# Kernel optimization log

Hardware: AMD Instinct MI355X
Metric: run time of the kernel (lower is better)

## Reference

```python
import jax, jax.numpy as jnp
import numpy as np
import math

N_NODES, N_EDGES, NNZ, D, L = 100000, 20000, 500000, 128, 4
ALPHA, LAMDA = 0.1, 0.5


def setup_inputs() -> dict:
    key = jax.random.key(0)
    ks = jax.random.split(key, 16)
    x = jax.random.normal(ks[0], (N_NODES, D), jnp.float32)
    e = jax.random.normal(ks[1], (N_EDGES, D), jnp.float32)
    nodes = jax.random.randint(ks[2], (NNZ,), 0, N_NODES)
    edges = jnp.sort(jax.random.randint(ks[3], (NNZ,), 0, N_EDGES)).at[-1].set(N_EDGES - 1)
    hyperedge_index = jnp.stack([nodes, edges]).astype(jnp.int32)
    dist_v2e = jax.random.randint(ks[4], (NNZ,), 0, 64).astype(jnp.float32)
    deg_v2e = jax.random.randint(ks[5], (NNZ,), 0, 64).astype(jnp.float32)
    dist_e2v = jax.random.randint(ks[6], (NNZ,), 0, 64).astype(jnp.float32)
    deg_e2v = jax.random.randint(ks[7], (NNZ,), 0, 64).astype(jnp.float32)
    s = 0.05
    W0 = jax.random.normal(ks[8], (D, D), jnp.float32) * s
    b0 = jnp.zeros((D,), jnp.float32)
    Wn = jax.random.normal(ks[9], (L, D, D), jnp.float32) * s
    We = jax.random.normal(ks[10], (L, D, D), jnp.float32) * s
    attn_w = jax.random.normal(ks[11], (L, 2 * D), jnp.float32) * s
    attn_b = jnp.zeros((L,), jnp.float32)
    wd_w = jax.random.normal(ks[12], (L,), jnp.float32) * s
    wd_b = jnp.zeros((L,), jnp.float32)
    wg_w = jax.random.normal(ks[13], (L,), jnp.float32) * s
    wg_b = jnp.zeros((L,), jnp.float32)
    return dict(x=x, e=e, hyperedge_index=hyperedge_index, dist_v2e=dist_v2e,
                deg_v2e=deg_v2e, dist_e2v=dist_e2v, deg_e2v=deg_e2v,
                W0=W0, b0=b0, Wn=Wn, We=We, attn_w=attn_w, attn_b=attn_b,
                wd_w=wd_w, wd_b=wd_b, wg_w=wg_w, wg_b=wg_b)


def _seg_softmax(s, idx, num):
    # numerically-stable scatter_softmax over segments idx
    m = jax.ops.segment_max(s, idx, num_segments=num)
    ex = jnp.exp(s - m[idx])
    den = jax.ops.segment_sum(ex, idx, num_segments=num)
    return ex / den[idx]


def _forward(x, e, hei, dv2e, gv2e, de2v, ge2v, W0, b0, Wn, We, aw, ab, wdw, wdb, wgw, wgb):
    nodes, edges = hei[0], hei[1]
    N, E = x.shape[0], e.shape[0]
    ones = jnp.ones(nodes.shape[0], x.dtype)
    dV = jax.ops.segment_sum(ones, nodes, num_segments=N)
    cnt = jax.ops.segment_sum(ones, edges, num_segments=E)
    dE = jax.ops.segment_sum(dV[nodes], edges, num_segments=E) / jnp.maximum(cnt, 1.0)
    degV = jnp.where(dV > 0, dV ** -0.5, 1.0)[:, None]   # [N,1]
    degE = jnp.where(dE > 0, dE ** -0.5, 1.0)[:, None]   # [E,1]

    x = jax.nn.relu(x @ W0 + b0)
    x0, e0 = x, e
    d = x.shape[1]
    for i in range(L):
        beta = math.log(LAMDA / (i + 1) + 1.0)
        # v2e attention: concat [x[nodes], e[edges]] -> softmax over edge segments
        sx1 = x @ aw[i, :d]; se1 = e @ aw[i, d:]
        s_v2e = sx1[nodes] + se1[edges] + ab[i] + dv2e * wdw[i] + wdb[i] + gv2e * wgw[i] + wgb[i]
        a_v2e = _seg_softmax(s_v2e, edges, E)[:, None]
        # e2v attention (flipped): concat [e[edges], x[nodes]] -> softmax over node segments
        se2 = e @ aw[i, :d]; sx2 = x @ aw[i, d:]
        s_e2v = se2[edges] + sx2[nodes] + ab[i] + de2v * wdw[i] + wdb[i] + ge2v * wgw[i] + wgb[i]
        a_e2v = _seg_softmax(s_e2v, nodes, N)[:, None]

        Xe1 = jax.ops.segment_sum(x[nodes] * a_v2e, edges, num_segments=E) * degE
        Xv1 = jax.ops.segment_sum(Xe1[edges] * a_e2v, nodes, num_segments=N) * degV
        Xv2 = jax.ops.segment_sum(e[edges] * a_e2v, nodes, num_segments=N) * degV
        Xe2 = jax.ops.segment_sum(Xv2[nodes] * a_v2e, edges, num_segments=E) * degE
        xm = (Xv1 + Xv2) * 0.5
        em = (Xe1 + Xe2) * 0.5
        xi = (1 - ALPHA) * xm + ALPHA * x0
        x = (1 - beta) * xi + beta * (xi @ Wn[i])
        ei = (1 - ALPHA) * em + ALPHA * e0
        e = (1 - beta) * ei + beta * (ei @ We[i])
        if i < L - 1:
            x = jax.nn.relu(x)
            e = jax.nn.relu(e)
    return x, e


def reference(x, e, hyperedge_index, dist_v2e, deg_v2e, dist_e2v, deg_e2v,
              W0, b0, Wn, We, attn_w, attn_b, wd_w, wd_b, wg_w, wg_b):
    return _forward(x, e, hyperedge_index, dist_v2e, deg_v2e, dist_e2v, deg_e2v,
                    W0, b0, Wn, We, attn_w, attn_b, wd_w, wd_b, wg_w, wg_b)
```

## Files before the change

kernel.cpp:

```cpp
#include <hip/hip_runtime.h>
#include <hip/hip_fp16.h>
#include <math.h>

#define DD 128
#define SCAN_BLOCKS 256
#define SMAX_CAP 128

typedef _Float16 f16x8 __attribute__((ext_vector_type(8)));
typedef float f32x4 __attribute__((ext_vector_type(4)));

__device__ inline float wave_sum(float v){
#pragma unroll
  for (int m = 32; m >= 1; m >>= 1) v += __shfl_xor(v, m, 64);
  return v;
}
__device__ inline int wave_sum_i(int v){
#pragma unroll
  for (int m = 32; m >= 1; m >>= 1) v += __shfl_xor(v, m, 64);
  return v;
}


__global__ void k_edge_offsets(const int* __restrict__ edges, int nnz, int E,
                               int* __restrict__ eo){
  int e = blockIdx.x * blockDim.x + threadIdx.x;
  if (e > E) return;
  int lo = 0, hi = nnz;
  while (lo < hi){ int mid = (lo + hi) >> 1; if (edges[mid] < e) lo = mid + 1; else hi = mid; }
  eo[e] = lo;
}

__global__ void k_hist(const int* __restrict__ nodes, int nnz, int* __restrict__ dV){
  int k = blockIdx.x * blockDim.x + threadIdx.x;
  if (k < nnz) atomicAdd(&dV[nodes[k]], 1);
}

__global__ __launch_bounds__(256) void k_scan_partial(const int* __restrict__ dV, int N,
                                                      int* __restrict__ part){
  int b = blockIdx.x, t = threadIdx.x;
  int chunk = (N + SCAN_BLOCKS - 1) / SCAN_BLOCKS;
  int s0 = b * chunk, s1 = min(s0 + chunk, N);
  int sum = 0;
  for (int n = s0 + t; n < s1; n += 256) sum += dV[n];
  sum = wave_sum_i(sum);
  __shared__ int wred[4];
  int lane = t & 63, wid = t >> 6;
  if (lane == 0) wred[wid] = sum;
  __syncthreads();
  if (t == 0) part[b] = wred[0] + wred[1] + wred[2] + wred[3];
}

__global__ __launch_bounds__(SCAN_BLOCKS) void k_scan_blocksums(int* __restrict__ part){
  __shared__ int sh[SCAN_BLOCKS];
  int t = threadIdx.x;
  int v = part[t];
  sh[t] = v; __syncthreads();
  for (int off = 1; off < SCAN_BLOCKS; off <<= 1){
    int add = (t >= off) ? sh[t - off] : 0;
    __syncthreads();
    sh[t] += add;
    __syncthreads();
  }
  part[t] = sh[t] - v;
}

__global__ __launch_bounds__(256) void k_scan_apply(const int* __restrict__ dV, int N, int nnz,
    const int* __restrict__ partScan, int* __restrict__ no, int* __restrict__ nfill,
    float* __restrict__ degV){
  int b = blockIdx.x, t = threadIdx.x;
  int chunk = (N + SCAN_BLOCKS - 1) / SCAN_BLOCKS;
  int s0 = b * chunk, s1 = min(s0 + chunk, N);
  int lane = t & 63, wid = t >> 6;
  __shared__ int wtot[4];
  __shared__ int s_run;
  if (t == 0) s_run = partScan[b];
  __syncthreads();
  for (int base = s0; base < s1; base += 256){
    int n = base + t;
    int d = (n < s1) ? dV[n] : 0;
    int v = d;
#pragma unroll
    for (int off = 1; off < 64; off <<= 1){
      int o = __shfl_up(v, off, 64);
      if (lane >= off) v += o;
    }
    if (lane == 63) wtot[wid] = v;
    __syncthreads();
    int run0 = s_run;
    int woff = 0;
    for (int w = 0; w < wid; w++) woff += wtot[w];
    if (n < s1){
      int excl = run0 + woff + v - d;
      no[n] = excl; nfill[n] = excl;
      degV[n] = d > 0 ? 1.0f / sqrtf((float)d) : 1.0f;
    }
    int btot = wtot[0] + wtot[1] + wtot[2] + wtot[3];
    __syncthreads();
    if (t == 0) s_run = run0 + btot;
    __syncthreads();
  }
  if (b == 0 && t == 0) no[N] = nnz;
}

__global__ void k_permpack(const int* __restrict__ nodes, const int* __restrict__ edges,
                           const float* __restrict__ dist, const float* __restrict__ deg,
                           int nnz, int* __restrict__ nfill, float2* __restrict__ pack){
  int k = blockIdx.x * blockDim.x + threadIdx.x;
  if (k < nnz){
    int pos = atomicAdd(&nfill[nodes[k]], 1);
    pack[pos] = make_float2(__int_as_float(edges[k]), dist[k] + 64.f * deg[k]);
  }
}

__global__ void k_edge_deg(const int* __restrict__ nodes, const int* __restrict__ eo, int E,
                           const int* __restrict__ dV, float* __restrict__ degE){
  int e = blockIdx.x * blockDim.x + threadIdx.x;
  if (e >= E) return;
  int b = eo[e], en = eo[e + 1];
  float s = 0.f;
  for (int k = b; k < en; k++) s += (float)dV[nodes[k]];
  float cnt = (float)(en - b);
  float dE = s / fmaxf(cnt, 1.0f);
  degE[e] = dE > 0.f ? 1.0f / sqrtf(dE) : 1.0f;
}

__global__ __launch_bounds__(256) void k_einit(const float2* __restrict__ e_in2,
    const float* __restrict__ aw1, const float* __restrict__ aw2,
    int E, __half2* __restrict__ e0h,
    float* __restrict__ se1, float* __restrict__ se2){
  int wave = threadIdx.x >> 6, lane = threadIdx.x & 63;
  int e = blockIdx.x * 4 + wave;
  if (e >= E) return;
  float2 v = e_in2[(size_t)e * 64 + lane];
  e0h[(size_t)e * 64 + lane] = __floats2half2_rn(v.x, v.y);
  float2 a2v = ((const float2*)aw2)[lane];
  float2 a1v = ((const float2*)aw1)[lane];
  float s1 = v.x * a2v.x + v.y * a2v.y;
  float s2 = v.x * a1v.x + v.y * a1v.y;
  s1 = wave_sum(s1); s2 = wave_sum(s2);
  if (lane == 0){ se1[e] = s1; se2[e] = s2; }
}

__global__ void k_wcast(const float* __restrict__ W0, const float* __restrict__ Wn,
                        const float* __restrict__ We, _Float16* __restrict__ Wt){
  int idx = blockIdx.x * 256 + threadIdx.x;
  if (idx >= 9 * 16384) return;
  int m = idx >> 14, r = idx & 16383;
  int n = r >> 7, k = r & 127;
  float v;
  if (m == 0){
    v = W0[k * 128 + n];
  } else {
    int i = (m <= 4) ? m - 1 : m - 5;
    const float* src = (m <= 4) ? Wn + (size_t)i * 16384 : We + (size_t)i * 16384;
    float beta = logf(0.5f / (float)(i + 1) + 1.0f);
    v = beta * src[k * 128 + n] + ((n == k) ? (1.0f - beta) : 0.f);
  }
  Wt[(size_t)m * 16384 + n * 128 + k] = (_Float16)v;
}


__device__ inline void acc8h(const float4 q, float w, float* a){
  float2 h0 = __half22float2(*(const __half2*)&q.x);
  float2 h1 = __half22float2(*(const __half2*)&q.y);
  float2 h2v = __half22float2(*(const __half2*)&q.z);
  float2 h3 = __half22float2(*(const __half2*)&q.w);
  a[0] += w * h0.x; a[1] += w * h0.y; a[2] += w * h1.x; a[3] += w * h1.y;
  a[4] += w * h2v.x; a[5] += w * h2v.y; a[6] += w * h3.x; a[7] += w * h3.y;
}

__global__ __launch_bounds__(256) void k_sma1(
    const int* __restrict__ nodes, const int* __restrict__ eo,
    const float* __restrict__ sx1, const float* __restrict__ se1,
    const float* __restrict__ dist, const float* __restrict__ deg,
    const float* __restrict__ ab, const float* __restrict__ wdw, const float* __restrict__ wdb,
    const float* __restrict__ wgw, const float* __restrict__ wgb, int li,
    const float* __restrict__ degE, const float4* __restrict__ xh4,
    const _Float16* __restrict__ ehL,
    int E, float* __restrict__ a_v2e, float* __restrict__ esc, _Float16* __restrict__ ETraw){
  __shared__ float lw[4][SMAX_CAP];
  int lane = threadIdx.x & 63;
  int wave = threadIdx.x >> 6;
  int e = blockIdx.x * 4 + wave;
  if (e >= E) return;
  int b = eo[e], en = eo[e + 1];
  int l16 = lane & 15, q16 = lane >> 4;
  if (b >= en){
    if (lane == 0) esc[e] = 0.f;
    if (q16 == 0){
      f16x8 ehv = *(const f16x8*)(ehL + (size_t)e * 128 + 8 * l16);
      f16x8 o0, o1;
#pragma unroll
      for (int q = 0; q < 2; q++){
        o0[4 * q] = (_Float16)0.f; o0[4 * q + 1] = (_Float16)0.f;
        o0[4 * q + 2] = ehv[2 * q]; o0[4 * q + 3] = ehv[2 * q + 1];
        o1[4 * q] = (_Float16)0.f; o1[4 * q + 1] = (_Float16)0.f;
        o1[4 * q + 2] = ehv[2 * q + 4]; o1[4 * q + 3] = ehv[2 * q + 5];
      }
      _Float16* dst = ETraw + (size_t)e * 256 + 16 * l16;
      *(f16x8*)dst = o0; *(f16x8*)(dst + 8) = o1;
    }
    return;
  }
  float base = se1[e] + ab[li] + wdb[li] + wgb[li];
  float wd = wdw[li], wg = wgw[li];
  float m = -INFINITY;
  float sreg[2];
#pragma unroll
  for (int c = 0; c < 2; c++){
    int k = b + lane + 64 * c;
    if (k < en){
      float s = sx1[nodes[k]] + base + dist[k] * wd + deg[k] * wg;
      sreg[c] = s; m = fmaxf(m, s);
    }
  }
  for (int k = b + lane + SMAX_CAP; k < en; k += 64){
    float s = sx1[nodes[k]] + base + dist[k] * wd + deg[k] * wg;
    m = fmaxf(m, s);
  }
#pragma unroll
  for (int mm = 32; mm >= 1; mm >>= 1) m = fmaxf(m, __shfl_xor(m, mm, 64));
  float sum = 0.f;
#pragma unroll
  for (int c = 0; c < 2; c++){
    int k = b + lane + 64 * c;
    if (k < en){
      float ex = __expf(sreg[c] - m);
      a_v2e[k] = ex; lw[wave][lane + 64 * c] = ex; sum += ex;
    }
  }
  for (int k = b + lane + SMAX_CAP; k < en; k += 64){
    float s = sx1[nodes[k]] + base + dist[k] * wd + deg[k] * wg;
    float ex = __expf(s - m);
    a_v2e[k] = ex; sum += ex;
  }
#pragma unroll
  for (int mm = 32; mm >= 1; mm >>= 1) sum += __shfl_xor(sum, mm, 64);
  float sc = degE[e] / sum;
  if (lane == 0) esc[e] = sc;
  float a[8] = {0.f, 0.f, 0.f, 0.f, 0.f, 0.f, 0.f, 0.f};
  int k = b + q16;
  for (; k + 4 < en; k += 8){
    float w0 = (k - b < SMAX_CAP) ? lw[wave][k - b] : a_v2e[k];
    float w1 = (k + 4 - b < SMAX_CAP) ? lw[wave][k + 4 - b] : a_v2e[k + 4];
    int n0 = nodes[k], n1 = nodes[k + 4];
    float4 v0 = xh4[(size_t)n0 * 16 + l16];
    float4 v1 = xh4[(size_t)n1 * 16 + l16];
    acc8h(v0, w0, a); acc8h(v1, w1, a);
  }
  for (; k < en; k += 4){
    float w = (k - b < SMAX_CAP) ? lw[wave][k - b] : a_v2e[k];
    int n = nodes[k];
    float4 v = xh4[(size_t)n * 16 + l16];
    acc8h(v, w, a);
  }
#pragma unroll
  for (int j = 0; j < 8; j++){
    a[j] += __shfl_xor(a[j], 16, 64);
    a[j] += __shfl_xor(a[j], 32, 64);
  }
  if (q16 == 0){
    f16x8 ehv = *(const f16x8*)(ehL + (size_t)e * 128 + 8 * l16);
    f16x8 o0, o1;
#pragma unroll
    for (int q = 0; q < 2; q++){
      __half2 xa = __floats2half2_rn(a[2 * q] * sc, a[2 * q + 1] * sc);
      o0[4 * q] = ((_Float16*)&xa)[0]; o0[4 * q + 1] = ((_Float16*)&xa)[1];
      o0[4 * q + 2] = ehv[2 * q]; o0[4 * q + 3] = ehv[2 * q + 1];
      __half2 xb = __floats2half2_rn(a[2 * q + 4] * sc, a[2 * q + 5] * sc);
      o1[4 * q] = ((_Float16*)&xb)[0]; o1[4 * q + 1] = ((_Float16*)&xb)[1];
      o1[4 * q + 2] = ehv[2 * q + 4]; o1[4 * q + 3] = ehv[2 * q + 5];
    }
    _Float16* dst = ETraw + (size_t)e * 256 + 16 * l16;
    *(f16x8*)dst = o0; *(f16x8*)(dst + 8) = o1;
  }
}

__device__ inline void acc8(const float4 q, float w, float* a1, float* a2){
  float2 x0 = __half22float2(*(const __half2*)&q.x);
  float2 e0 = __half22float2(*(const __half2*)&q.y);
  float2 x1 = __half22float2(*(const __half2*)&q.z);
  float2 e1 = __half22float2(*(const __half2*)&q.w);
  a1[0] += w * x0.x; a1[1] += w * x0.y; a1[2] += w * x1.x; a1[3] += w * x1.y;
  a2[0] += w * e0.x; a2[1] += w * e0.y; a2[2] += w * e1.x; a2[3] += w * e1.y;
}

__global__ __launch_bounds__(256) void k_agg2f(
    const float2* __restrict__ pack, const int* __restrict__ no,
    const float* __restrict__ se2, const float* __restrict__ sx2,
    const float* __restrict__ ab, const float* __restrict__ wdw, const float* __restrict__ wdb,
    const float* __restrict__ wgw, const float* __restrict__ wgb, int li,
    const float4* __restrict__ ETq,
    const float* __restrict__ degV, const __half2* __restrict__ x0h,
    int N, __half2* __restrict__ Xv2h, __half2* __restrict__ xiH){
  int lane = threadIdx.x & 63;
  int wave = threadIdx.x >> 6;
  int l32 = lane & 31, half = lane >> 5;
  int n = blockIdx.x * 4 + wave;
  if (n >= N) return;
  int b = no[n], en = no[n + 1];
  float base = sx2[n] + ab[li] + wdb[li] + wgb[li];
  float wd = wdw[li], wg = wgw[li];
  float2 x0v2 = *(const float2*)&x0h[(size_t)n * 64 + 2 * l32];
  float l_run = 0.f;
  float a1[4] = {0.f, 0.f, 0.f, 0.f}, a2[4] = {0.f, 0.f, 0.f, 0.f};
  if (en - b <= 32){
    int cs = en - b;
    float s = -INFINITY; int e_l = 0;
    if (l32 < cs){
      float2 pk = pack[b + l32];
      e_l = __float_as_int(pk.x);
      int vi = (int)pk.y;
      s = se2[e_l] + base + (float)(vi & 63) * wd + (float)(vi >> 6) * wg;
    }
    float m_c = s;
#pragma unroll
    for (int mm = 16; mm >= 1; mm >>= 1) m_c = fmaxf(m_c, __shfl_xor(m_c, mm, 32));
    float p = (l32 < cs) ? __expf(s - m_c) : 0.f;
    l_run = p;
#pragma unroll
    for (int mm = 16; mm >= 1; mm >>= 1) l_run += __shfl_xor(l_run, mm, 32);
    int jj = 0;
    for (; jj + 3 < cs; jj += 4){
      int i0 = jj + half, i1 = jj + 2 + half;
      float w0 = __shfl(p, i0, 32), w1 = __shfl(p, i1, 32);
      int e0i = __shfl(e_l, i0, 32), e1i = __shfl(e_l, i1, 32);
      float4 q0 = ETq[(size_t)e0i * 32 + l32];
      float4 q1 = ETq[(size_t)e1i * 32 + l32];
      acc8(q0, w0, a1, a2);
      acc8(q1, w1, a1, a2);
    }
    for (; jj < cs; jj += 2){
      int idx = jj + half;
      int idxc = min(idx, cs - 1);
      float wr = __shfl(p, idxc, 32);
      int er = __shfl(e_l, idxc, 32);
      float w = (idx < cs) ? wr : 0.f;
      float4 q = ETq[(size_t)er * 32 + l32];
      acc8(q, w, a1, a2);
    }
  } else {
    float m_run = -INFINITY;
    for (int cb = b; cb < en; cb += 32){
      int cs = min(32, en - cb);
      float s = -INFINITY; int e_l = 0;
      if (l32 < cs){
        float2 pk = pack[cb + l32];
        e_l = __float_as_int(pk.x);
        int vi = (int)pk.y;
        s = se2[e_l] + base + (float)(vi & 63) * wd + (float)(vi >> 6) * wg;
      }
      float m_c = s;
#pragma unroll
      for (int mm = 16; mm >= 1; mm >>= 1) m_c = fmaxf(m_c, __shfl_xor(m_c, mm, 32));
      float p = (l32 < cs) ? __expf(s - m_c) : 0.f;
      float l_c = p;
#pragma unroll
      for (int mm = 16; mm >= 1; mm >>= 1) l_c += __shfl_xor(l_c, mm, 32);
      float m_new = fmaxf(m_run, m_c);
      float f_old = __expf(m_run - m_new);
      float f_c = __expf(m_c - m_new);
#pragma unroll
      for (int r = 0; r < 4; r++){ a1[r] *= f_old; a2[r] *= f_old; }
      l_run = l_run * f_old + l_c * f_c;
      m_run = m_new;
      int jj = 0;
      for (; jj + 3 < cs; jj += 4){
        int i0 = jj + half, i1 = jj + 2 + half;
        float w0 = __shfl(p, i0, 32) * f_c, w1 = __shfl(p, i1, 32) * f_c;
        int e0i = __shfl(e_l, i0, 32), e1i = __shfl(e_l, i1, 32);
        float4 q0 = ETq[(size_t)e0i * 32 + l32];
        float4 q1 = ETq[(size_t)e1i * 32 + l32];
        acc8(q0, w0, a1, a2);
        acc8(q1, w1, a1, a2);
      }
      for (; jj < cs; jj += 2){
        int idx = jj + half;
        int idxc = min(idx, cs - 1);
        float wr = __shfl(p, idxc, 32);
        int er = __shfl(e_l, idxc, 32);
        float w = (idx < cs) ? wr * f_c : 0.f;
        float4 q = ETq[(size_t)er * 32 + l32];
        acc8(q, w, a1, a2);
      }
    }
  }
#pragma unroll
  for (int r = 0; r < 4; r++){
    a1[r] += __shfl_xor(a1[r], 32, 64);
    a2[r] += __shfl_xor(a2[r], 32, 64);
  }
  if (half == 0){
    float inv = l_run > 0.f ? 1.0f / l_run : 0.f;
    float dv = degV[n] * inv;
    float2 st;
    *(__half2*)&st.x = __floats2half2_rn(a2[0] * dv, a2[1] * dv);
    *(__half2*)&st.y = __floats2half2_rn(a2[2] * dv, a2[3] * dv);
    *(float2*)&Xv2h[(size_t)n * 64 + 2 * l32] = st;
    float2 h0 = __half22float2(*(const __half2*)&x0v2.x);
    float2 h1 = __half22float2(*(const __half2*)&x0v2.y);
    float2 xo;
    *(__half2*)&xo.x = __floats2half2_rn(0.45f * dv * (a1[0] + a2[0]) + 0.1f * h0.x,
                                         0.45f * dv * (a1[1] + a2[1]) + 0.1f * h0.y);
    *(__half2*)&xo.y = __floats2half2_rn(0.45f * dv * (a1[2] + a2[2]) + 0.1f * h1.x,
                                         0.45f * dv * (a1[3] + a2[3]) + 0.1f * h1.y);
    *(float2*)&xiH[(size_t)n * 64 + 2 * l32] = xo;
  }
}

__global__ __launch_bounds__(256) void k_agg3(const int* __restrict__ nodes, const int* __restrict__ eo,
    const float4* __restrict__ Xv2h4, const float* __restrict__ a_v2e, const float* __restrict__ esc,
    const float4* __restrict__ ETq, const float4* __restrict__ e0h4,
    int E, __half2* __restrict__ eiH){
  int lane = threadIdx.x & 63;
  int wave = threadIdx.x >> 6;
  int e = blockIdx.x * 4 + wave;
  if (e >= E) return;
  int b = eo[e], en = eo[e + 1];
  int l16 = lane & 15, q16 = lane >> 4;
  float a[8] = {0.f, 0.f, 0.f, 0.f, 0.f, 0.f, 0.f, 0.f};
  int k = b + q16;
  for (; k + 4 < en; k += 8){
    float w0 = a_v2e[k], w1 = a_v2e[k + 4];
    int n0 = nodes[k], n1 = nodes[k + 4];
    float4 v0 = Xv2h4[(size_t)n0 * 16 + l16];
    float4 v1 = Xv2h4[(size_t)n1 * 16 + l16];
    acc8h(v0, w0, a); acc8h(v1, w1, a);
  }
  for (; k < en; k += 4){
    float w = a_v2e[k];
    int n = nodes[k];
    float4 v = Xv2h4[(size_t)n * 16 + l16];
    acc8h(v, w, a);
  }
#pragma unroll
  for (int j = 0; j < 8; j++){
    a[j] += __shfl_xor(a[j], 16, 64);
    a[j] += __shfl_xor(a[j], 32, 64);
  }
  if (q16 == 0){
    float dE = esc[e];
    float4 q0 = ETq[(size_t)e * 32 + 2 * l16];
    float4 q1 = ETq[(size_t)e * 32 + 2 * l16 + 1];
    float2 x01 = __half22float2(*(const __half2*)&q0.x);
    float2 x23 = __half22float2(*(const __half2*)&q0.z);
    float2 x45 = __half22float2(*(const __half2*)&q1.x);
    float2 x67 = __half22float2(*(const __half2*)&q1.z);
    float4 ev = e0h4[(size_t)e * 16 + l16];
    float2 g0 = __half22float2(*(const __half2*)&ev.x);
    float2 g1 = __half22float2(*(const __half2*)&ev.y);
    float2 g2 = __half22float2(*(const __half2*)&ev.z);
    float2 g3 = __half22float2(*(const __half2*)&ev.w);
    float4 o;
    *(__half2*)&o.x = __floats2half2_rn(0.45f * (x01.x + a[0] * dE) + 0.1f * g0.x,
                                        0.45f * (x01.y + a[1] * dE) + 0.1f * g0.y);
    *(__half2*)&o.y = __floats2half2_rn(0.45f * (x23.x + a[2] * dE) + 0.1f * g1.x,
                                        0.45f * (x23.y + a[3] * dE) + 0.1f * g1.y);
    *(__half2*)&o.z = __floats2half2_rn(0.45f * (x45.x + a[4] * dE) + 0.1f * g2.x,
                                        0.45f * (x45.y + a[5] * dE) + 0.1f * g2.y);
    *(__half2*)&o.w = __floats2half2_rn(0.45f * (x67.x + a[6] * dE) + 0.1f * g3.x,
                                        0.45f * (x67.y + a[7] * dE) + 0.1f * g3.y);
    *(float4*)&eiH[(size_t)e * 64 + 4 * l16] = o;
  }
}

__device__ __forceinline__ void gemm_body(
    const _Float16* __restrict__ Ah, const _Float16* __restrict__ Wt,
    float* __restrict__ outf, _Float16* __restrict__ outh,
    const float* __restrict__ awA, const float* __restrict__ awB,
    float* __restrict__ sA, float* __restrict__ sB,
    int nrows, int do_relu, int blockRow0, _Float16 (*sh)[136]){
  int lane = threadIdx.x & 63, wave = threadIdx.x >> 6;
  int row0 = blockRow0 + wave * 16;
  int lm = lane & 15;
  int lk8 = (lane >> 4) * 8;
  int rbase = (lane >> 4) * 4;
  if (row0 < nrows){
    int arow = row0 + lm; if (arow >= nrows) arow = nrows - 1;
    f16x8 afrag[4];
#pragma unroll
    for (int ks = 0; ks < 4; ks++)
      afrag[ks] = *(const f16x8*)(Ah + (size_t)arow * 128 + ks * 32 + lk8);
    float da[4] = {0.f, 0.f, 0.f, 0.f}, db[4] = {0.f, 0.f, 0.f, 0.f};
    for (int t = 0; t < 8; t++){
      f32x4 acc = {0.f, 0.f, 0.f, 0.f};
#pragma unroll
      for (int ks = 0; ks < 4; ks++){
        f16x8 bf = *(const f16x8*)(Wt + (size_t)(t * 16 + lm) * 128 + ks * 32 + lk8);
        acc = __builtin_amdgcn_mfma_f32_16x16x32_f16(afrag[ks], bf, acc, 0, 0, 0);
      }
      int col = t * 16 + lm;
      float wa = 0.f, wb = 0.f;
      if (awA){ wa = awA[col]; wb = awB[col]; }
#pragma unroll
      for (int r = 0; r < 4; r++){
        int gr = row0 + rbase + r;
        float v = acc[r];
        if (do_relu) v = fmaxf(v, 0.f);
        if (outf && gr < nrows) outf[(size_t)gr * 128 + col] = v;
        if (outh) sh[wave * 16 + rbase + r][col] = (_Float16)v;
        if (gr < nrows){ da[r] += v * wa; db[r] += v * wb; }
      }
    }
    if (awA){
#pragma unroll
      for (int r = 0; r < 4; r++){
        float a = da[r], bb = db[r];
#pragma unroll
        for (int m = 8; m >= 1; m >>= 1){
          a += __shfl_xor(a, m, 64);
          bb += __shfl_xor(bb, m, 64);
        }
        int gr = row0 + rbase + r;
        if (lm == 0 && gr < nrows){ sA[gr] = a; sB[gr] = bb; }
      }
    }
  }
  if (outh){
    __syncthreads();
    for (int i = threadIdx.x; i < 64 * 16; i += 256){
      int rr = i >> 4, cc = (i & 15) * 8;
      int gr = blockRow0 + rr;
      if (gr < nrows)
        *(f16x8*)(outh + (size_t)gr * 128 + cc) = *(const f16x8*)&sh[rr][cc];
    }
  }
}

__global__ __launch_bounds__(256) void k_gemm2(
    const _Float16* __restrict__ Ax, const _Float16* __restrict__ Wx,
    const _Float16* __restrict__ Ae, const _Float16* __restrict__ Wte,
    float* __restrict__ outfx, _Float16* __restrict__ outhx,
    float* __restrict__ outfe, _Float16* __restrict__ outhe,
    const float* __restrict__ awAx, const float* __restrict__ awBx,
    float* __restrict__ sAx, float* __restrict__ sBx,
    const float* __restrict__ awAe, const float* __restrict__ awBe,
    float* __restrict__ sAe, float* __restrict__ sBe,
    int nrx, int nre, int nbx, int do_relu){
  __shared__ _Float16 sh[64][136];
  if ((int)blockIdx.x < nbx){
    gemm_body(Ax, Wx, outfx, outhx, awAx, awBx, sAx, sBx, nrx, do_relu,
              blockIdx.x * 64, sh);
  } else {
    gemm_body(Ae, Wte, outfe, outhe, awAe, awBe, sAe, sBe, nre, do_relu,
              (blockIdx.x - nbx) * 64, sh);
  }
}

__global__ __launch_bounds__(256) void k_gemm0(
    const float* __restrict__ Af, const _Float16* __restrict__ Wt,
    const float* __restrict__ bias,
    _Float16* __restrict__ outh, _Float16* __restrict__ outh2,
    const float* __restrict__ awA, const float* __restrict__ awB,
    float* __restrict__ sA, float* __restrict__ sB, int nrows){
  __shared__ _Float16 sh[64][136];
  int wave = threadIdx.x >> 6, lane = threadIdx.x & 63;
  int blockRow0 = blockIdx.x * 64;
  int row0 = blockRow0 + wave * 16;
  int lm = lane & 15;
  int lk8 = (lane >> 4) * 8;
  int rbase = (lane >> 4) * 4;
  if (row0 < nrows){
    int arow = row0 + lm; if (arow >= nrows) arow = nrows - 1;
    const float* ap = Af + (size_t)arow * 128;
    f16x8 afrag[4];
#pragma unroll
    for (int ks = 0; ks < 4; ks++){
      float4 v0 = *(const float4*)(ap + ks * 32 + lk8);
      float4 v1 = *(const float4*)(ap + ks * 32 + lk8 + 4);
      f16x8 a;
      a[0] = (_Float16)v0.x; a[1] = (_Float16)v0.y; a[2] = (_Float16)v0.z; a[3] = (_Float16)v0.w;
      a[4] = (_Float16)v1.x; a[5] = (_Float16)v1.y; a[6] = (_Float16)v1.z; a[7] = (_Float16)v1.w;
      afrag[ks] = a;
    }
    float da[4] = {0.f, 0.f, 0.f, 0.f}, db[4] = {0.f, 0.f, 0.f, 0.f};
    for (int t = 0; t < 8; t++){
      f32x4 acc = {0.f, 0.f, 0.f, 0.f};
#pragma unroll
      for (int ks = 0; ks < 4; ks++){
        f16x8 bf = *(const f16x8*)(Wt + (size_t)(t * 16 + lm) * 128 + ks * 32 + lk8);
        acc = __builtin_amdgcn_mfma_f32_16x16x32_f16(afrag[ks], bf, acc, 0, 0, 0);
      }
      int col = t * 16 + lm;
      float wa = awA[col], wb = awB[col];
      float bi = bias[col];
#pragma unroll
      for (int r = 0; r < 4; r++){
        int gr = row0 + rbase + r;
        float v = fmaxf(acc[r] + bi, 0.f);
        sh[wave * 16 + rbase + r][col] = (_Float16)v;
        if (gr < nrows){ da[r] += v * wa; db[r] += v * wb; }
      }
    }
#pragma unroll
    for (int r = 0; r < 4; r++){
      float a = da[r], bb = db[r];
#pragma unroll
      for (int m = 8; m >= 1; m >>= 1){
        a += __shfl_xor(a, m, 64);
        bb += __shfl_xor(bb, m, 64);
      }
      int gr = row0 + rbase + r;
      if (lm == 0 && gr < nrows){ sA[gr] = a; sB[gr] = bb; }
    }
  }
  __syncthreads();
  for (int i = threadIdx.x; i < 64 * 16; i += 256){
    int rr = i >> 4, cc = (i & 15) * 8;
    int gr = blockRow0 + rr;
    if (gr < nrows){
      f16x8 v = *(const f16x8*)&sh[rr][cc];
      *(f16x8*)(outh + (size_t)gr * 128 + cc) = v;
      *(f16x8*)(outh2 + (size_t)gr * 128 + cc) = v;
    }
  }
}


extern "C" void kernel_launch(void* const* d_in, const int* in_sizes, int n_in,
                              void* d_out, int out_size, void* d_ws, size_t ws_size,
                              hipStream_t stream) {
  const float* x_in     = (const float*)d_in[0];
  const float* e_in     = (const float*)d_in[1];
  const int*   hei      = (const int*)d_in[2];
  const float* dist_v2e = (const float*)d_in[3];
  const float* deg_v2e  = (const float*)d_in[4];
  const float* dist_e2v = (const float*)d_in[5];
  const float* deg_e2v  = (const float*)d_in[6];
  const float* W0       = (const float*)d_in[7];
  const float* b0       = (const float*)d_in[8];
  const float* Wn       = (const float*)d_in[9];
  const float* We       = (const float*)d_in[10];
  const float* attn_w   = (const float*)d_in[11];
  const float* attn_b   = (const float*)d_in[12];
  const float* wd_w     = (const float*)d_in[13];
  const float* wd_b     = (const float*)d_in[14];
  const float* wg_w     = (const float*)d_in[15];
  const float* wg_b     = (const float*)d_in[16];

  const int N   = in_sizes[0] / DD;
  const int E   = in_sizes[1] / DD;
  const int NNZ = in_sizes[2] / 2;
  const int* nodesArr = hei;
  const int* edgesArr = hei + NNZ;

  float* out_x = (float*)d_out;
  float* out_e = (float*)d_out + (size_t)N * DD;

  __half2* xh   = (__half2*)((char*)out_x + (size_t)N * DD * 2);
  _Float16* ETraw = (_Float16*)out_e;
  const float4* ETq = (const float4*)out_e;

  char* wsp = (char*)d_ws;
  auto alloc = [&](size_t bytes) -> void* {
    void* p = (void*)wsp;
    wsp += (bytes + 255) / 256 * 256;
    return p;
  };
  _Float16* x0h  = (_Float16*)alloc((size_t)N * DD * 2);
  _Float16* Xv2h = (_Float16*)alloc((size_t)N * DD * 2);
  _Float16* xiH  = (_Float16*)alloc((size_t)N * DD * 2);
  _Float16* eiH  = (_Float16*)alloc((size_t)E * DD * 2);
  _Float16* e0h  = (_Float16*)alloc((size_t)E * DD * 2);
  _Float16* ehL  = (_Float16*)alloc((size_t)E * DD * 2);
  _Float16* Wt   = (_Float16*)alloc((size_t)9 * 16384 * 2);
  float* sx1   = (float*)alloc((size_t)N * 4);
  float* sx2   = (float*)alloc((size_t)N * 4);
  float* se1   = (float*)alloc((size_t)E * 4);
  float* se2   = (float*)alloc((size_t)E * 4);
  float* a_v2e = (float*)alloc((size_t)NNZ * 4);
  float* degV  = (float*)alloc((size_t)N * 4);
  float* degE  = (float*)alloc((size_t)E * 4);
  float* esc   = (float*)alloc((size_t)E * 4);
  float2* pack = (float2*)alloc((size_t)NNZ * 8);
  int* dV_i  = (int*)alloc((size_t)N * 4);
  int* no_   = (int*)alloc((size_t)(N + 1) * 4);
  int* nfill = (int*)alloc((size_t)N * 4);
  int* eo    = (int*)alloc((size_t)(E + 1) * 4);
  int* part  = (int*)alloc((size_t)SCAN_BLOCKS * 4);

  hipMemsetAsync(dV_i, 0, (size_t)N * 4, stream);
  k_edge_offsets<<<(E + 1 + 255) / 256, 256, 0, stream>>>(edgesArr, NNZ, E, eo);
  k_hist<<<(NNZ + 255) / 256, 256, 0, stream>>>(nodesArr, NNZ, dV_i);
  k_scan_partial<<<SCAN_BLOCKS, 256, 0, stream>>>(dV_i, N, part);
  k_scan_blocksums<<<1, SCAN_BLOCKS, 0, stream>>>(part);
  k_scan_apply<<<SCAN_BLOCKS, 256, 0, stream>>>(dV_i, N, NNZ, part, no_, nfill, degV);
  k_permpack<<<(NNZ + 255) / 256, 256, 0, stream>>>(nodesArr, edgesArr, dist_e2v, deg_e2v,
                                                    NNZ, nfill, pack);
  k_edge_deg<<<(E + 255) / 256, 256, 0, stream>>>(nodesArr, eo, E, dV_i, degE);
  k_wcast<<<(9 * 16384 + 255) / 256, 256, 0, stream>>>(W0, Wn, We, Wt);

  const float* aw1_0 = attn_w;
  const float* aw2_0 = attn_w + 128;

  k_einit<<<(E + 3) / 4, 256, 0, stream>>>((const float2*)e_in, aw1_0, aw2_0,
                                            E, (__half2*)e0h, se1, se2);

  k_gemm0<<<(N + 63) / 64, 256, 0, stream>>>(x_in, Wt, b0,
      (_Float16*)xh, x0h, aw1_0, aw2_0, sx1, sx2, N);

  const int nbx = (N + 63) / 64, nbe = (E + 63) / 64;
  for (int i = 0; i < 4; i++){
    const float* aw1n = (i < 3) ? attn_w + (size_t)(i + 1) * 256        : nullptr;
    const float* aw2n = (i < 3) ? attn_w + (size_t)(i + 1) * 256 + 128  : nullptr;
    const _Float16* ehCur = (i == 0) ? e0h : ehL;

    k_sma1<<<(E + 3) / 4, 256, 0, stream>>>(nodesArr, eo, sx1, se1,
        dist_v2e, deg_v2e, attn_b, wd_w, wd_b, wg_w, wg_b, i, degE,
        (const float4*)xh, ehCur, E, a_v2e, esc, ETraw);

    k_agg2f<<<(N + 3) / 4, 256, 0, stream>>>(pack, no_, se2, sx2,
        attn_b, wd_w, wd_b, wg_w, wg_b, i,
        ETq, degV, (const __half2*)x0h, N, (__half2*)Xv2h, (__half2*)xiH);

    k_agg3<<<(E + 3) / 4, 256, 0, stream>>>(nodesArr, eo, (const float4*)Xv2h,
        a_v2e, esc, ETq, (const float4*)e0h, E, (__half2*)eiH);

    k_gemm2<<<nbx + nbe, 256, 0, stream>>>(
        xiH, Wt + (size_t)(1 + i) * 16384,
        eiH, Wt + (size_t)(5 + i) * 16384,
        (i == 3) ? out_x : nullptr, (i < 3) ? (_Float16*)xh : nullptr,
        (i == 3) ? out_e : nullptr, (i < 3) ? ehL : nullptr,
        aw1n, aw2n, sx1, sx2,
        aw2n, aw1n, se1, se2,
        N, E, nbx, i < 3 ? 1 : 0);
  }
}
```

Before: 821.5 us.

## Co-schedule node GEMM with edge aggregation and use 32-lane groups in agg2f

```diff
diff --git a/kernel.cpp b/kernel.cpp
--- a/kernel.cpp
+++ b/kernel.cpp
@@ -293,10 +293,9 @@
     const float4* __restrict__ ETq,
     const float* __restrict__ degV, const __half2* __restrict__ x0h,
     int N, __half2* __restrict__ Xv2h, __half2* __restrict__ xiH){
-  int lane = threadIdx.x & 63;
-  int wave = threadIdx.x >> 6;
-  int l32 = lane & 31, half = lane >> 5;
-  int n = blockIdx.x * 4 + wave;
+  int l32 = threadIdx.x & 31;
+  int grp = threadIdx.x >> 5;
+  int n = blockIdx.x * 8 + grp;
   if (n >= N) return;
   int b = no[n], en = no[n + 1];
   float base = sx2[n] + ab[li] + wdb[li] + wgb[li];
@@ -321,22 +320,34 @@
 #pragma unroll
     for (int mm = 16; mm >= 1; mm >>= 1) l_run += __shfl_xor(l_run, mm, 32);
     int jj = 0;
+    for (; jj + 7 < cs; jj += 8){
+      float w[8]; int ei[8]; float4 q[8];
+#pragma unroll
+      for (int u = 0; u < 8; u++){
+        w[u] = __shfl(p, jj + u, 32);
+        ei[u] = __shfl(e_l, jj + u, 32);
+      }
+#pragma unroll
+      for (int u = 0; u < 8; u++) q[u] = ETq[(size_t)ei[u] * 32 + l32];
+#pragma unroll
+      for (int u = 0; u < 8; u++) acc8(q[u], w[u], a1, a2);
+    }
     for (; jj + 3 < cs; jj += 4){
-      int i0 = jj + half, i1 = jj + 2 + half;
-      float w0 = __shfl(p, i0, 32), w1 = __shfl(p, i1, 32);
-      int e0i = __shfl(e_l, i0, 32), e1i = __shfl(e_l, i1, 32);
-      float4 q0 = ETq[(size_t)e0i * 32 + l32];
-      float4 q1 = ETq[(size_t)e1i * 32 + l32];
-      acc8(q0, w0, a1, a2);
-      acc8(q1, w1, a1, a2);
-    }
-    for (; jj < cs; jj += 2){
-      int idx = jj + half;
-      int idxc = min(idx, cs - 1);
-      float wr = __shfl(p, idxc, 32);
-      int er = __shfl(e_l, idxc, 32);
-      float w = (idx < cs) ? wr : 0.f;
-      float4 q = ETq[(size_t)er * 32 + l32];
+      float w[4]; int ei[4]; float4 q[4];
+#pragma unroll
+      for (int u = 0; u < 4; u++){
+        w[u] = __shfl(p, jj + u, 32);
+        ei[u] = __shfl(e_l, jj + u, 32);
+      }
+#pragma unroll
+      for (int u = 0; u < 4; u++) q[u] = ETq[(size_t)ei[u] * 32 + l32];
+#pragma unroll
+      for (int u = 0; u < 4; u++) acc8(q[u], w[u], a1, a2);
+    }
+    for (; jj < cs; jj++){
+      float w = __shfl(p, jj, 32);
+      int ei_ = __shfl(e_l, jj, 32);
+      float4 q = ETq[(size_t)ei_ * 32 + l32];
       acc8(q, w, a1, a2);
     }
   } else {
@@ -366,55 +377,132 @@
       m_run = m_new;
       int jj = 0;
       for (; jj + 3 < cs; jj += 4){
-        int i0 = jj + half, i1 = jj + 2 + half;
-        float w0 = __shfl(p, i0, 32) * f_c, w1 = __shfl(p, i1, 32) * f_c;
-        int e0i = __shfl(e_l, i0, 32), e1i = __shfl(e_l, i1, 32);
+        float w0 = __shfl(p, jj, 32) * f_c;
+        float w1 = __shfl(p, jj + 1, 32) * f_c;
+        float w2 = __shfl(p, jj + 2, 32) * f_c;
+        float w3 = __shfl(p, jj + 3, 32) * f_c;
+        int e0i = __shfl(e_l, jj, 32);
+        int e1i = __shfl(e_l, jj + 1, 32);
+        int e2i = __shfl(e_l, jj + 2, 32);
+        int e3i = __shfl(e_l, jj + 3, 32);
         float4 q0 = ETq[(size_t)e0i * 32 + l32];
         float4 q1 = ETq[(size_t)e1i * 32 + l32];
+        float4 q2 = ETq[(size_t)e2i * 32 + l32];
+        float4 q3 = ETq[(size_t)e3i * 32 + l32];
         acc8(q0, w0, a1, a2);
         acc8(q1, w1, a1, a2);
-      }
-      for (; jj < cs; jj += 2){
-        int idx = jj + half;
-        int idxc = min(idx, cs - 1);
-        float wr = __shfl(p, idxc, 32);
-        int er = __shfl(e_l, idxc, 32);
-        float w = (idx < cs) ? wr * f_c : 0.f;
-        float4 q = ETq[(size_t)er * 32 + l32];
+        acc8(q2, w2, a1, a2);
+        acc8(q3, w3, a1, a2);
+      }
+      for (; jj < cs; jj++){
+        float w = __shfl(p, jj, 32) * f_c;
+        int ei_ = __shfl(e_l, jj, 32);
+        float4 q = ETq[(size_t)ei_ * 32 + l32];
         acc8(q, w, a1, a2);
       }
     }
   }
-#pragma unroll
-  for (int r = 0; r < 4; r++){
-    a1[r] += __shfl_xor(a1[r], 32, 64);
-    a2[r] += __shfl_xor(a2[r], 32, 64);
-  }
-  if (half == 0){
-    float inv = l_run > 0.f ? 1.0f / l_run : 0.f;
-    float dv = degV[n] * inv;
-    float2 st;
-    *(__half2*)&st.x = __floats2half2_rn(a2[0] * dv, a2[1] * dv);
-    *(__half2*)&st.y = __floats2half2_rn(a2[2] * dv, a2[3] * dv);
-    *(float2*)&Xv2h[(size_t)n * 64 + 2 * l32] = st;
-    float2 h0 = __half22float2(*(const __half2*)&x0v2.x);
-    float2 h1 = __half22float2(*(const __half2*)&x0v2.y);
-    float2 xo;
-    *(__half2*)&xo.x = __floats2half2_rn(0.45f * dv * (a1[0] + a2[0]) + 0.1f * h0.x,
-                                         0.45f * dv * (a1[1] + a2[1]) + 0.1f * h0.y);
-    *(__half2*)&xo.y = __floats2half2_rn(0.45f * dv * (a1[2] + a2[2]) + 0.1f * h1.x,
-                                         0.45f * dv * (a1[3] + a2[3]) + 0.1f * h1.y);
-    *(float2*)&xiH[(size_t)n * 64 + 2 * l32] = xo;
-  }
-}
-
-__global__ __launch_bounds__(256) void k_agg3(const int* __restrict__ nodes, const int* __restrict__ eo,
-    const float4* __restrict__ Xv2h4, const float* __restrict__ a_v2e, const float* __restrict__ esc,
+  float inv = l_run > 0.f ? 1.0f / l_run : 0.f;
+  float dv = degV[n] * inv;
+  float2 st;
+  *(__half2*)&st.x = __floats2half2_rn(a2[0] * dv, a2[1] * dv);
+  *(__half2*)&st.y = __floats2half2_rn(a2[2] * dv, a2[3] * dv);
+  *(float2*)&Xv2h[(size_t)n * 64 + 2 * l32] = st;
+  float2 h0 = __half22float2(*(const __half2*)&x0v2.x);
+  float2 h1 = __half22float2(*(const __half2*)&x0v2.y);
+  float2 xo;
+  *(__half2*)&xo.x = __floats2half2_rn(0.45f * dv * (a1[0] + a2[0]) + 0.1f * h0.x,
+                                       0.45f * dv * (a1[1] + a2[1]) + 0.1f * h0.y);
+  *(__half2*)&xo.y = __floats2half2_rn(0.45f * dv * (a1[2] + a2[2]) + 0.1f * h1.x,
+                                       0.45f * dv * (a1[3] + a2[3]) + 0.1f * h1.y);
+  *(float2*)&xiH[(size_t)n * 64 + 2 * l32] = xo;
+}
+
+__device__ __forceinline__ void gemm_body(
+    const _Float16* __restrict__ Ah, const _Float16* __restrict__ Wt,
+    float* __restrict__ outf, _Float16* __restrict__ outh,
+    const float* __restrict__ awA, const float* __restrict__ awB,
+    float* __restrict__ sA, float* __restrict__ sB,
+    int nrows, int do_relu, int blockRow0, _Float16 (*sh)[136]){
+  int lane = threadIdx.x & 63, wave = threadIdx.x >> 6;
+  int row0 = blockRow0 + wave * 16;
+  int lm = lane & 15;
+  int lk8 = (lane >> 4) * 8;
+  int rbase = (lane >> 4) * 4;
+  if (row0 < nrows){
+    int arow = row0 + lm; if (arow >= nrows) arow = nrows - 1;
+    f16x8 afrag[4];
+#pragma unroll
+    for (int ks = 0; ks < 4; ks++)
+      afrag[ks] = *(const f16x8*)(Ah + (size_t)arow * 128 + ks * 32 + lk8);
+    float da[4] = {0.f, 0.f, 0.f, 0.f}, db[4] = {0.f, 0.f, 0.f, 0.f};
+    for (int t = 0; t < 8; t++){
+      f32x4 acc = {0.f, 0.f, 0.f, 0.f};
+#pragma unroll
+      for (int ks = 0; ks < 4; ks++){
+        f16x8 bf = *(const f16x8*)(Wt + (size_t)(t * 16 + lm) * 128 + ks * 32 + lk8);
+        acc = __builtin_amdgcn_mfma_f32_16x16x32_f16(afrag[ks], bf, acc, 0, 0, 0);
+      }
+      int col = t * 16 + lm;
+      float wa = 0.f, wb = 0.f;
+      if (awA){ wa = awA[col]; wb = awB[col]; }
+#pragma unroll
+      for (int r = 0; r < 4; r++){
+        int gr = row0 + rbase + r;
+        float v = acc[r];
+        if (do_relu) v = fmaxf(v, 0.f);
+        if (outf && gr < nrows) outf[(size_t)gr * 128 + col] = v;
+        if (outh) sh[wave * 16 + rbase + r][col] = (_Float16)v;
+        if (gr < nrows){ da[r] += v * wa; db[r] += v * wb; }
+      }
+    }
+    if (awA){
+#pragma unroll
+      for (int r = 0; r < 4; r++){
+        float a = da[r], bb = db[r];
+#pragma unroll
+        for (int m = 8; m >= 1; m >>= 1){
+          a += __shfl_xor(a, m, 64);
+          bb += __shfl_xor(bb, m, 64);
+        }
+        int gr = row0 + rbase + r;
+        if (lm == 0 && gr < nrows){ sA[gr] = a; sB[gr] = bb; }
+      }
+    }
+  }
+  if (outh){
+    __syncthreads();
+    for (int i = threadIdx.x; i < 64 * 16; i += 256){
+      int rr = i >> 4, cc = (i & 15) * 8;
+      int gr = blockRow0 + rr;
+      if (gr < nrows)
+        *(f16x8*)(outh + (size_t)gr * 128 + cc) = *(const f16x8*)&sh[rr][cc];
+    }
+  }
+}
+
+__global__ __launch_bounds__(256) void k_a3gx(
+    const int* __restrict__ nodes, const int* __restrict__ eo,
+    const float4* __restrict__ Xv2h4, const float* __restrict__ a_v2e,
+    const float* __restrict__ esc,
     const float4* __restrict__ ETq, const float4* __restrict__ e0h4,
-    int E, __half2* __restrict__ eiH){
+    int E, __half2* __restrict__ eiH, int nbx,
+    const _Float16* __restrict__ Ah, const _Float16* __restrict__ Wt,
+    float* __restrict__ outf, _Float16* __restrict__ outh,
+    const float* __restrict__ awA, const float* __restrict__ awB,
+    float* __restrict__ sA, float* __restrict__ sB, int N, int do_relu){
+  __shared__ _Float16 sh[64][136];
+  int g = blockIdx.x;
+  int k4 = g >> 2, r4 = g & 3;
+  bool isx = (r4 == 3) && (k4 < nbx);
+  if (isx){
+    gemm_body(Ah, Wt, outf, outh, awA, awB, sA, sB, N, do_relu, k4 * 64, sh);
+    return;
+  }
+  int axi = g - min(k4 + (r4 == 3 ? 1 : 0), nbx);
   int lane = threadIdx.x & 63;
   int wave = threadIdx.x >> 6;
-  int e = blockIdx.x * 4 + wave;
+  int e = axi * 4 + wave;
   if (e >= E) return;
   int b = eo[e], en = eo[e + 1];
   int l16 = lane & 15, q16 = lane >> 4;
@@ -464,87 +552,14 @@
   }
 }
 
-__device__ __forceinline__ void gemm_body(
+__global__ __launch_bounds__(256) void k_gemme(
     const _Float16* __restrict__ Ah, const _Float16* __restrict__ Wt,
     float* __restrict__ outf, _Float16* __restrict__ outh,
     const float* __restrict__ awA, const float* __restrict__ awB,
-    float* __restrict__ sA, float* __restrict__ sB,
-    int nrows, int do_relu, int blockRow0, _Float16 (*sh)[136]){
-  int lane = threadIdx.x & 63, wave = threadIdx.x >> 6;
-  int row0 = blockRow0 + wave * 16;
-  int lm = lane & 15;
-  int lk8 = (lane >> 4) * 8;
-  int rbase = (lane >> 4) * 4;
-  if (row0 < nrows){
-    int arow = row0 + lm; if (arow >= nrows) arow = nrows - 1;
-    f16x8 afrag[4];
-#pragma unroll
-    for (int ks = 0; ks < 4; ks++)
-      afrag[ks] = *(const f16x8*)(Ah + (size_t)arow * 128 + ks * 32 + lk8);
-    float da[4] = {0.f, 0.f, 0.f, 0.f}, db[4] = {0.f, 0.f, 0.f, 0.f};
-    for (int t = 0; t < 8; t++){
-      f32x4 acc = {0.f, 0.f, 0.f, 0.f};
-#pragma unroll
-      for (int ks = 0; ks < 4; ks++){
-        f16x8 bf = *(const f16x8*)(Wt + (size_t)(t * 16 + lm) * 128 + ks * 32 + lk8);
-        acc = __builtin_amdgcn_mfma_f32_16x16x32_f16(afrag[ks], bf, acc, 0, 0, 0);
-      }
-      int col = t * 16 + lm;
-      float wa = 0.f, wb = 0.f;
-      if (awA){ wa = awA[col]; wb = awB[col]; }
-#pragma unroll
-      for (int r = 0; r < 4; r++){
-        int gr = row0 + rbase + r;
-        float v = acc[r];
-        if (do_relu) v = fmaxf(v, 0.f);
-        if (outf && gr < nrows) outf[(size_t)gr * 128 + col] = v;
-        if (outh) sh[wave * 16 + rbase + r][col] = (_Float16)v;
-        if (gr < nrows){ da[r] += v * wa; db[r] += v * wb; }
-      }
-    }
-    if (awA){
-#pragma unroll
-      for (int r = 0; r < 4; r++){
-        float a = da[r], bb = db[r];
-#pragma unroll
-        for (int m = 8; m >= 1; m >>= 1){
-          a += __shfl_xor(a, m, 64);
-          bb += __shfl_xor(bb, m, 64);
-        }
-        int gr = row0 + rbase + r;
-        if (lm == 0 && gr < nrows){ sA[gr] = a; sB[gr] = bb; }
-      }
-    }
-  }
-  if (outh){
-    __syncthreads();
-    for (int i = threadIdx.x; i < 64 * 16; i += 256){
-      int rr = i >> 4, cc = (i & 15) * 8;
-      int gr = blockRow0 + rr;
-      if (gr < nrows)
-        *(f16x8*)(outh + (size_t)gr * 128 + cc) = *(const f16x8*)&sh[rr][cc];
-    }
-  }
-}
-
-__global__ __launch_bounds__(256) void k_gemm2(
-    const _Float16* __restrict__ Ax, const _Float16* __restrict__ Wx,
-    const _Float16* __restrict__ Ae, const _Float16* __restrict__ Wte,
-    float* __restrict__ outfx, _Float16* __restrict__ outhx,
-    float* __restrict__ outfe, _Float16* __restrict__ outhe,
-    const float* __restrict__ awAx, const float* __restrict__ awBx,
-    float* __restrict__ sAx, float* __restrict__ sBx,
-    const float* __restrict__ awAe, const float* __restrict__ awBe,
-    float* __restrict__ sAe, float* __restrict__ sBe,
-    int nrx, int nre, int nbx, int do_relu){
+    float* __restrict__ sA, float* __restrict__ sB, int nrows, int do_relu){
   __shared__ _Float16 sh[64][136];
-  if ((int)blockIdx.x < nbx){
-    gemm_body(Ax, Wx, outfx, outhx, awAx, awBx, sAx, sBx, nrx, do_relu,
-              blockIdx.x * 64, sh);
-  } else {
-    gemm_body(Ae, Wte, outfe, outhe, awAe, awBe, sAe, sBe, nre, do_relu,
-              (blockIdx.x - nbx) * 64, sh);
-  }
+  gemm_body(Ah, Wt, outf, outh, awA, awB, sA, sB, nrows, do_relu,
+            blockIdx.x * 64, sh);
 }
 
 __global__ __launch_bounds__(256) void k_gemm0(
@@ -699,7 +714,7 @@
   k_gemm0<<<(N + 63) / 64, 256, 0, stream>>>(x_in, Wt, b0,
       (_Float16*)xh, x0h, aw1_0, aw2_0, sx1, sx2, N);
 
-  const int nbx = (N + 63) / 64, nbe = (E + 63) / 64;
+  const int nbx = (N + 63) / 64, nbe = (E + 63) / 64, nbA = (E + 3) / 4;
   for (int i = 0; i < 4; i++){
     const float* aw1n = (i < 3) ? attn_w + (size_t)(i + 1) * 256        : nullptr;
     const float* aw2n = (i < 3) ? attn_w + (size_t)(i + 1) * 256 + 128  : nullptr;
@@ -709,20 +724,19 @@
         dist_v2e, deg_v2e, attn_b, wd_w, wd_b, wg_w, wg_b, i, degE,
         (const float4*)xh, ehCur, E, a_v2e, esc, ETraw);
 
-    k_agg2f<<<(N + 3) / 4, 256, 0, stream>>>(pack, no_, se2, sx2,
+    k_agg2f<<<(N + 7) / 8, 256, 0, stream>>>(pack, no_, se2, sx2,
         attn_b, wd_w, wd_b, wg_w, wg_b, i,
         ETq, degV, (const __half2*)x0h, N, (__half2*)Xv2h, (__half2*)xiH);
 
-    k_agg3<<<(E + 3) / 4, 256, 0, stream>>>(nodesArr, eo, (const float4*)Xv2h,
-        a_v2e, esc, ETq, (const float4*)e0h, E, (__half2*)eiH);
-
-    k_gemm2<<<nbx + nbe, 256, 0, stream>>>(
+    k_a3gx<<<nbA + nbx, 256, 0, stream>>>(
+        nodesArr, eo, (const float4*)Xv2h, a_v2e, esc, ETq, (const float4*)e0h,
+        E, (__half2*)eiH, nbx,
         xiH, Wt + (size_t)(1 + i) * 16384,
-        eiH, Wt + (size_t)(5 + i) * 16384,
         (i == 3) ? out_x : nullptr, (i < 3) ? (_Float16*)xh : nullptr,
+        aw1n, aw2n, sx1, sx2, N, i < 3 ? 1 : 0);
+
+    k_gemme<<<nbe, 256, 0, stream>>>(eiH, Wt + (size_t)(5 + i) * 16384,
         (i == 3) ? out_e : nullptr, (i < 3) ? ehL : nullptr,
-        aw1n, aw2n, sx1, sx2,
-        aw2n, aw1n, se1, se2,
-        N, E, nbx, i < 3 ? 1 : 0);
-  }
-}
+        aw2n, aw1n, se1, se2, E, i < 3 ? 1 : 0);
+  }
+}
```

After: 1.053 ms. 1.28x slower.
